# Kernel optimization log

Hardware: AMD Instinct MI355X
Metric: run time of the kernel (lower is better)

The kernel has to match this reference:

```python
import jax, jax.numpy as jnp
import numpy as np

B, S, HID = 1, 2048, 1024
NH, NKV, HD = 16, 4, 64
SCALING = 0.125  # attention_multiplier = 1/sqrt(head_dim)
ROPE_THETA = 10000.0
NEG_MIN = jnp.finfo(jnp.float32).min


def rotate_half(x):
    x1, x2 = jnp.split(x, 2, axis=-1)
    return jnp.concatenate([-x2, x1], axis=-1)


def setup_inputs() -> dict:
    key = jax.random.key(0)
    ks = jax.random.split(key, 6)
    hidden_states = jax.random.normal(ks[0], (B, S, HID), dtype=jnp.float32)
    # RoPE tables: [1, 1, S, HD]
    inv_freq = 1.0 / (ROPE_THETA ** (np.arange(0, HD, 2, dtype=np.float32) / HD))
    t = np.arange(S, dtype=np.float32)
    freqs = np.outer(t, inv_freq)                      # [S, HD/2]
    emb = np.concatenate([freqs, freqs], axis=-1)      # [S, HD]
    cos = jnp.asarray(np.cos(emb))[None, None]
    sin = jnp.asarray(np.sin(emb))[None, None]
    attention_mask = jnp.ones((B, S), dtype=bool)
    sc = 0.02
    Wq = jax.random.normal(ks[1], (HID, NH * HD), dtype=jnp.float32) * sc
    Wk = jax.random.normal(ks[2], (HID, NKV * HD), dtype=jnp.float32) * sc
    Wv = jax.random.normal(ks[3], (HID, NKV * HD), dtype=jnp.float32) * sc
    Wo = jax.random.normal(ks[4], (NH * HD, HID), dtype=jnp.float32) * sc
    return {"hidden_states": hidden_states, "cos": cos, "sin": sin,
            "attention_mask": attention_mask, "Wq": Wq, "Wk": Wk, "Wv": Wv, "Wo": Wo}


def reference(hidden_states, cos, sin, attention_mask, Wq, Wk, Wv, Wo):
    b, s, _ = hidden_states.shape
    # projections -> [B, H, S, D]
    q = (hidden_states @ Wq).reshape(b, s, NH, HD).transpose(0, 2, 1, 3)
    k = (hidden_states @ Wk).reshape(b, s, NKV, HD).transpose(0, 2, 1, 3)
    v = (hidden_states @ Wv).reshape(b, s, NKV, HD).transpose(0, 2, 1, 3)
    # RoPE (full head_dim rotation; cos/sin broadcast over batch/heads)
    q = q * cos + rotate_half(q) * sin
    k = k * cos + rotate_half(k) * sin
    # repeat_kv: expand kv heads to match query heads
    n_rep = NH // NKV
    k = jnp.repeat(k, n_rep, axis=1)
    v = jnp.repeat(v, n_rep, axis=1)
    # scores: [B, H, Sq, Sk]
    attn = jnp.einsum('bhqd,bhkd->bhqk', q, k) * SCALING
    mask = attention_mask[:, None, None, :].astype(attn.dtype)  # bool padding mask
    attn = attn + (1.0 - mask) * NEG_MIN
    attn = jax.nn.softmax(attn.astype(jnp.float32), axis=-1).astype(q.dtype)
    out = jnp.einsum('bhqk,bhkd->bhqd', attn, v)
    out = out.transpose(0, 2, 1, 3).reshape(b, s, NH * HD)
    return out @ Wo
```

## Files before the change

kernel.cpp:

```cpp
#include <hip/hip_runtime.h>
#include <stdint.h>

typedef __attribute__((ext_vector_type(8))) short short8;
typedef __attribute__((ext_vector_type(4))) short short4v;
typedef __attribute__((ext_vector_type(4))) float floatx4;

#define AS1 __attribute__((address_space(1)))
#define AS3 __attribute__((address_space(3)))

__device__ __forceinline__ void async16(const void* g, void* l) {
  __builtin_amdgcn_global_load_lds((const AS1 unsigned int*)g, (AS3 unsigned int*)l, 16, 0, 0);
}

__device__ __forceinline__ short f2bf(float f) {
  unsigned u = __float_as_uint(f);
  u = (u + 0x7FFF + ((u >> 16) & 1)) >> 16;
  return (short)u;
}

__device__ __forceinline__ void stage_sw(const short* src, int stride,
                                         short* tile, int cb, int lane) {
  int i = cb + lane;
  int r = i >> 3, j = i & 7;
  async16(src + (size_t)r * stride + ((j ^ (r & 7)) * 8), tile + cb * 8);
}
__device__ __forceinline__ int sw(int row, int c8) {
  return row * 64 + ((c8 ^ (row & 7)) * 8);
}

__global__ void k_f2bf(const float* __restrict__ in, short* __restrict__ out, int n) {
  int i = (blockIdx.x * 256 + threadIdx.x) * 4;
  if (i < n) {
    floatx4 v = *(const floatx4*)(in + i);
    short4v o;
    o.x = f2bf(v.x); o.y = f2bf(v.y); o.z = f2bf(v.z); o.w = f2bf(v.w);
    *(short4v*)(out + i) = o;
  }
}

__global__ void k_wt(const float* __restrict__ W, short* __restrict__ Wt, int K, int N) {
  __shared__ short t[32][33];
  int k0 = blockIdx.y * 32, n0 = blockIdx.x * 32;
  int tx = threadIdx.x, ty = threadIdx.y;
#pragma unroll
  for (int i = 0; i < 4; i++)
    t[ty + 8 * i][tx] = f2bf(W[(size_t)(k0 + ty + 8 * i) * N + n0 + tx]);
  __syncthreads();
#pragma unroll
  for (int i = 0; i < 4; i++)
    Wt[(size_t)(n0 + ty + 8 * i) * K + k0 + tx] = t[tx][ty + 8 * i];
}

__global__ void k_rope(const float* __restrict__ src, int stride, int off,
                       short* __restrict__ dst, const float* __restrict__ cosp,
                       const float* __restrict__ sinp, int H, int S, float scale) {
  int tid = blockIdx.x * 256 + threadIdx.x;
  int d = tid & 63;
  int h = (tid >> 6) % H;
  int s = tid / (64 * H);
  float v = src[(size_t)s * stride + off + h * 64 + d];
  float o = src[(size_t)s * stride + off + h * 64 + (d ^ 32)];
  float rot = (d < 32) ? -o : o;
  float c = cosp[s * 64 + d], sn = sinp[s * 64 + d];
  dst[((size_t)h * S + s) * 64 + d] = f2bf((v * c + rot * sn) * scale);
}

__global__ void k_vt(const float* __restrict__ src, short* __restrict__ Vt, int S) {
  __shared__ short t[32][33];
  int s0 = blockIdx.x * 32;
  int d0 = blockIdx.y * 32;
  int h = blockIdx.z;
  int tx = threadIdx.x, ty = threadIdx.y;
#pragma unroll
  for (int i = 0; i < 4; i++)
    t[ty + 8 * i][tx] = f2bf(src[(size_t)(s0 + ty + 8 * i) * 1536 + 1280 + h * 64 + d0 + tx]);
  __syncthreads();
#pragma unroll
  for (int i = 0; i < 4; i++)
    Vt[((size_t)h * 64 + d0 + ty + 8 * i) * S + s0 + tx] = t[tx][ty + 8 * i];
}

__global__ __launch_bounds__(256) void k_gemm(const short* __restrict__ A,
                                              const short* __restrict__ Bt,
                                              float* __restrict__ C,
                                              int M, int N, int K) {
  int tid = threadIdx.x;
  int w = tid >> 6, lane = tid & 63, quad = lane >> 4, l16 = lane & 15;
  __shared__ short As[64 * 64];
  __shared__ short Bs[128 * 64];
  const short* Ag = A + (size_t)(blockIdx.y * 64) * K;
  const short* Bg = Bt + (size_t)(blockIdx.x * 128) * K;
  floatx4 acc[4][2] = {};
  for (int kk = 0; kk < K; kk += 64) {
    __syncthreads();
#pragma unroll
    for (int t = 0; t < 2; t++) stage_sw(Ag + kk, K, As, (w * 2 + t) * 64, lane);
#pragma unroll
    for (int t = 0; t < 4; t++) stage_sw(Bg + kk, K, Bs, (w * 4 + t) * 64, lane);
    __syncthreads();
#pragma unroll
    for (int ks = 0; ks < 2; ks++) {
      short8 af[4], bfr[2];
#pragma unroll
      for (int i = 0; i < 4; i++)
        af[i] = *(const short8*)&As[sw(i * 16 + l16, ks * 4 + quad)];
#pragma unroll
      for (int j = 0; j < 2; j++)
        bfr[j] = *(const short8*)&Bs[sw(w * 32 + j * 16 + l16, ks * 4 + quad)];
#pragma unroll
      for (int i = 0; i < 4; i++)
#pragma unroll
        for (int j = 0; j < 2; j++)
          acc[i][j] = __builtin_amdgcn_mfma_f32_16x16x32_bf16(af[i], bfr[j], acc[i][j], 0, 0, 0);
    }
  }
#pragma unroll
  for (int i = 0; i < 4; i++)
#pragma unroll
    for (int j = 0; j < 2; j++)
#pragma unroll
      for (int r = 0; r < 4; r++) {
        int row = blockIdx.y * 64 + i * 16 + quad * 4 + r;
        int col = blockIdx.x * 128 + w * 32 + j * 16 + l16;
        C[(size_t)row * N + col] = acc[i][j][r];
      }
}

__global__ __launch_bounds__(256) void k_attn(const short* __restrict__ Qb,
                                              const short* __restrict__ Kb,
                                              const short* __restrict__ Vt,
                                              short* __restrict__ AOb) {
  int qt = blockIdx.x;
  int h = blockIdx.y;
  int kvh = h >> 2;
  int tid = threadIdx.x, w = tid >> 6, lane = tid & 63, quad = lane >> 4, l16 = lane & 15;
  __shared__ short Qs[4096];
  __shared__ short Ks[2][4096];
  __shared__ short Vs[2][4096];
  __shared__ short Ps[4][1152];
  const short* Qg = Qb + ((size_t)h * 2048 + qt * 64) * 64;
  const short* Kg0 = Kb + (size_t)kvh * 2048 * 64;
  const short* Vg0 = Vt + (size_t)kvh * 64 * 2048;
#pragma unroll
  for (int t = 0; t < 2; t++) stage_sw(Qg, 64, Qs, (w * 2 + t) * 64, lane);
#pragma unroll
  for (int t = 0; t < 2; t++) stage_sw(Kg0, 64, Ks[0], (w * 2 + t) * 64, lane);
#pragma unroll
  for (int t = 0; t < 2; t++) stage_sw(Vg0, 2048, Vs[0], (w * 2 + t) * 64, lane);
  short8 qf[2];
  floatx4 accO[4] = {};
  float lsum = 0.f;
  short* myPs = Ps[w];
  for (int kt = 0; kt < 32; kt++) {
    __syncthreads();
    if (kt == 0) {
      qf[0] = *(const short8*)&Qs[sw(w * 16 + l16, quad)];
      qf[1] = *(const short8*)&Qs[sw(w * 16 + l16, 4 + quad)];
    }
    if (kt + 1 < 32) {
      int nb = (kt + 1) & 1;
#pragma unroll
      for (int t = 0; t < 2; t++)
        stage_sw(Kg0 + (kt + 1) * 4096, 64, Ks[nb], (w * 2 + t) * 64, lane);
#pragma unroll
      for (int t = 0; t < 2; t++)
        stage_sw(Vg0 + (kt + 1) * 64, 2048, Vs[nb], (w * 2 + t) * 64, lane);
    }
    int cbuf = kt & 1;
    floatx4 accS[4] = {};
#pragma unroll
    for (int ks = 0; ks < 2; ks++)
#pragma unroll
      for (int mt = 0; mt < 4; mt++) {
        short8 af = *(const short8*)&Ks[cbuf][sw(mt * 16 + l16, ks * 4 + quad)];
        accS[mt] = __builtin_amdgcn_mfma_f32_16x16x32_bf16(af, qf[ks], accS[mt], 0, 0, 0);
      }
#pragma unroll
    for (int mt = 0; mt < 4; mt++) {
      short4v pk;
#pragma unroll
      for (int r = 0; r < 4; r++) {
        float p = __builtin_amdgcn_exp2f(accS[mt][r]);
        lsum += p;
        pk[r] = f2bf(p);
      }
      *(short4v*)&myPs[l16 * 72 + mt * 16 + quad * 4] = pk;
    }
    asm volatile("s_waitcnt lgkmcnt(0)" ::: "memory");
#pragma unroll
    for (int ks = 0; ks < 2; ks++) {
      short8 pf = *(const short8*)&myPs[l16 * 72 + ks * 32 + quad * 8];
#pragma unroll
      for (int dt = 0; dt < 4; dt++) {
        short8 vf = *(const short8*)&Vs[cbuf][sw(dt * 16 + l16, ks * 4 + quad)];
        accO[dt] = __builtin_amdgcn_mfma_f32_16x16x32_bf16(pf, vf, accO[dt], 0, 0, 0);
      }
    }
  }
  float ls = lsum;
  ls += __shfl_xor(ls, 16);
  ls += __shfl_xor(ls, 32);
  float inv[4];
#pragma unroll
  for (int r = 0; r < 4; r++)
    inv[r] = 1.0f / __shfl(ls, (lane & 48) | (quad * 4 + r));
#pragma unroll
  for (int dt = 0; dt < 4; dt++)
#pragma unroll
    for (int r = 0; r < 4; r++) {
      int srow = qt * 64 + w * 16 + quad * 4 + r;
      int col = h * 64 + dt * 16 + l16;
      AOb[(size_t)srow * 1024 + col] = f2bf(accO[dt][r] * inv[r]);
    }
}

extern "C" void kernel_launch(void* const* d_in, const int* in_sizes, int n_in,
                              void* d_out, int out_size, void* d_ws, size_t ws_size,
                              hipStream_t stream) {
  const float* X    = (const float*)d_in[0];
  const float* cosp = (const float*)d_in[1];
  const float* sinp = (const float*)d_in[2];
  const float* Wq = (const float*)d_in[4];
  const float* Wk = (const float*)d_in[5];
  const float* Wv = (const float*)d_in[6];
  const float* Wo = (const float*)d_in[7];
  float* out = (float*)d_out;

  short* Xb   = (short*)d_ws;
  short* Wqt  = Xb + 2097152;
  short* Wkt  = Wqt + 1048576;
  short* Wvt  = Wkt + 262144;
  short* Wot  = Wvt + 262144;
  float* QKVf = (float*)(Wot + 1048576);
  short* Qb2  = (short*)(QKVf + 3145728);
  short* Kb2  = Qb2 + 2097152;
  short* Vtb  = Kb2 + 524288;
  short* AOb  = Vtb + 524288;

  const float QSCALE = 0.125f * 1.44269504088896340736f;
  dim3 tb(32, 8);

  k_f2bf<<<2048, 256, 0, stream>>>(X, Xb, 2097152);
  k_wt<<<dim3(32, 32), tb, 0, stream>>>(Wq, Wqt, 1024, 1024);
  k_wt<<<dim3(8, 32), tb, 0, stream>>>(Wk, Wkt, 1024, 256);
  k_wt<<<dim3(8, 32), tb, 0, stream>>>(Wv, Wvt, 1024, 256);
  k_wt<<<dim3(32, 32), tb, 0, stream>>>(Wo, Wot, 1024, 1024);
  k_gemm<<<dim3(12, 32), 256, 0, stream>>>(Xb, Wqt, QKVf, 2048, 1536, 1024);
  k_rope<<<8192, 256, 0, stream>>>(QKVf, 1536, 0, Qb2, cosp, sinp, 16, 2048, QSCALE);
  k_rope<<<2048, 256, 0, stream>>>(QKVf, 1536, 1024, Kb2, cosp, sinp, 4, 2048, 1.0f);
  k_vt<<<dim3(64, 2, 4), tb, 0, stream>>>(QKVf, Vtb, 2048);
  k_attn<<<dim3(32, 16), 256, 0, stream>>>(Qb2, Kb2, Vtb, AOb);
  k_gemm<<<dim3(8, 32), 256, 0, stream>>>(AOb, Wot, out, 2048, 1024, 1024);
}
```

Before: 169.1 us.

## Fuse prep kernels, fold RoPE and V transpose into QKV GEMM, widen attention tiles

Merges the X conversion and four weight-transpose launches into one prep kernel. RoPE, Q scaling and the V transpose now run in the QKV GEMM epilogue, using a remapped B-tile row order so each lane holds both halves of a head dimension pair. This removes the fp32 QKV intermediate round trip and several launches. Attention now gives each wave 32 query rows loaded straight into registers, which halves the grid and K/V restaging per query but raises register pressure and lowers block count.

```diff
diff --git a/kernel.cpp b/kernel.cpp
--- a/kernel.cpp
+++ b/kernel.cpp
@@ -28,56 +28,107 @@
   return row * 64 + ((c8 ^ (row & 7)) * 8);
 }
 
-__global__ void k_f2bf(const float* __restrict__ in, short* __restrict__ out, int n) {
-  int i = (blockIdx.x * 256 + threadIdx.x) * 4;
-  if (i < n) {
-    floatx4 v = *(const floatx4*)(in + i);
+__global__ void k_prep(const float* __restrict__ X, const float* __restrict__ Wq,
+                       const float* __restrict__ Wk, const float* __restrict__ Wv,
+                       const float* __restrict__ Wo, short* __restrict__ Xb,
+                       short* __restrict__ Wqkvt, short* __restrict__ Wot) {
+  int b = blockIdx.x, tid = threadIdx.x;
+  if (b < 2048) {
+    int i = b * 1024 + tid * 4;
+    floatx4 v = *(const floatx4*)(X + i);
     short4v o;
     o.x = f2bf(v.x); o.y = f2bf(v.y); o.z = f2bf(v.z); o.w = f2bf(v.w);
-    *(short4v*)(out + i) = o;
-  }
-}
-
-__global__ void k_wt(const float* __restrict__ W, short* __restrict__ Wt, int K, int N) {
+    *(short4v*)(Xb + i) = o;
+    return;
+  }
+  const float* src; short* dst; int N, brel, rowoff;
+  if (b < 3072)      { src = Wq; dst = Wqkvt; N = 1024; brel = b - 2048; rowoff = 0; }
+  else if (b < 3328) { src = Wk; dst = Wqkvt; N = 256;  brel = b - 3072; rowoff = 1024; }
+  else if (b < 3584) { src = Wv; dst = Wqkvt; N = 256;  brel = b - 3328; rowoff = 1280; }
+  else               { src = Wo; dst = Wot;   N = 1024; brel = b - 3584; rowoff = 0; }
   __shared__ short t[32][33];
-  int k0 = blockIdx.y * 32, n0 = blockIdx.x * 32;
-  int tx = threadIdx.x, ty = threadIdx.y;
+  int nt = N >> 5;
+  int n0 = (brel % nt) * 32, k0 = (brel / nt) * 32;
+  int tx = tid & 31, ty = tid >> 5;
 #pragma unroll
   for (int i = 0; i < 4; i++)
-    t[ty + 8 * i][tx] = f2bf(W[(size_t)(k0 + ty + 8 * i) * N + n0 + tx]);
+    t[ty + 8 * i][tx] = f2bf(src[(size_t)(k0 + ty + 8 * i) * N + n0 + tx]);
   __syncthreads();
 #pragma unroll
   for (int i = 0; i < 4; i++)
-    Wt[(size_t)(n0 + ty + 8 * i) * K + k0 + tx] = t[tx][ty + 8 * i];
-}
-
-__global__ void k_rope(const float* __restrict__ src, int stride, int off,
-                       short* __restrict__ dst, const float* __restrict__ cosp,
-                       const float* __restrict__ sinp, int H, int S, float scale) {
-  int tid = blockIdx.x * 256 + threadIdx.x;
-  int d = tid & 63;
-  int h = (tid >> 6) % H;
-  int s = tid / (64 * H);
-  float v = src[(size_t)s * stride + off + h * 64 + d];
-  float o = src[(size_t)s * stride + off + h * 64 + (d ^ 32)];
-  float rot = (d < 32) ? -o : o;
-  float c = cosp[s * 64 + d], sn = sinp[s * 64 + d];
-  dst[((size_t)h * S + s) * 64 + d] = f2bf((v * c + rot * sn) * scale);
-}
-
-__global__ void k_vt(const float* __restrict__ src, short* __restrict__ Vt, int S) {
-  __shared__ short t[32][33];
-  int s0 = blockIdx.x * 32;
-  int d0 = blockIdx.y * 32;
-  int h = blockIdx.z;
-  int tx = threadIdx.x, ty = threadIdx.y;
-#pragma unroll
-  for (int i = 0; i < 4; i++)
-    t[ty + 8 * i][tx] = f2bf(src[(size_t)(s0 + ty + 8 * i) * 1536 + 1280 + h * 64 + d0 + tx]);
-  __syncthreads();
-#pragma unroll
-  for (int i = 0; i < 4; i++)
-    Vt[((size_t)h * 64 + d0 + ty + 8 * i) * S + s0 + tx] = t[tx][ty + 8 * i];
+    dst[(size_t)(rowoff + n0 + ty + 8 * i) * 1024 + k0 + tx] = t[tx][ty + 8 * i];
+}
+
+__global__ __launch_bounds__(256) void k_gemmqkv(const short* __restrict__ A,
+                                                 const short* __restrict__ Bt,
+                                                 short* __restrict__ Qb,
+                                                 short* __restrict__ Kb,
+                                                 short* __restrict__ Vtb,
+                                                 const float* __restrict__ cosp,
+                                                 const float* __restrict__ sinp,
+                                                 float qscale) {
+  int tid = threadIdx.x;
+  int w = tid >> 6, lane = tid & 63, quad = lane >> 4, l16 = lane & 15;
+  __shared__ short As[64 * 64];
+  __shared__ short Bs[128 * 64];
+  const int K = 1024;
+  const short* Ag = A + (size_t)(blockIdx.y * 64) * K;
+  const short* Bg = Bt + (size_t)(blockIdx.x * 128) * K;
+  int hw = w & 1;
+  int dlo = (w >> 1) * 16 + l16;
+  floatx4 acc[4][2] = {};
+  for (int kk = 0; kk < K; kk += 64) {
+    __syncthreads();
+#pragma unroll
+    for (int t = 0; t < 2; t++) stage_sw(Ag + kk, K, As, (w * 2 + t) * 64, lane);
+#pragma unroll
+    for (int t = 0; t < 4; t++) stage_sw(Bg + kk, K, Bs, (w * 4 + t) * 64, lane);
+    __syncthreads();
+#pragma unroll
+    for (int ks = 0; ks < 2; ks++) {
+      short8 af[4], bfr[2];
+#pragma unroll
+      for (int i = 0; i < 4; i++)
+        af[i] = *(const short8*)&As[sw(i * 16 + l16, ks * 4 + quad)];
+#pragma unroll
+      for (int j = 0; j < 2; j++)
+        bfr[j] = *(const short8*)&Bs[sw(hw * 64 + j * 32 + (w >> 1) * 16 + l16, ks * 4 + quad)];
+#pragma unroll
+      for (int i = 0; i < 4; i++)
+#pragma unroll
+        for (int j = 0; j < 2; j++)
+          acc[i][j] = __builtin_amdgcn_mfma_f32_16x16x32_bf16(af[i], bfr[j], acc[i][j], 0, 0, 0);
+    }
+  }
+  int bx = blockIdx.x, by = blockIdx.y;
+  if (bx < 10) {
+    short* dst; float scale;
+    if (bx < 8) { dst = Qb + (size_t)(bx * 2 + hw) * 2048 * 64; scale = qscale; }
+    else        { dst = Kb + (size_t)((bx - 8) * 2 + hw) * 2048 * 64; scale = 1.0f; }
+#pragma unroll
+    for (int i = 0; i < 4; i++)
+#pragma unroll
+      for (int r = 0; r < 4; r++) {
+        int s = by * 64 + i * 16 + quad * 4 + r;
+        float c = cosp[s * 64 + dlo], sn = sinp[s * 64 + dlo];
+        float v0 = acc[i][0][r], v1 = acc[i][1][r];
+        dst[(size_t)s * 64 + dlo]      = f2bf((v0 * c - v1 * sn) * scale);
+        dst[(size_t)s * 64 + 32 + dlo] = f2bf((v1 * c + v0 * sn) * scale);
+      }
+  } else {
+    short* dst = Vtb + (size_t)((bx - 10) * 2 + hw) * 64 * 2048;
+#pragma unroll
+    for (int j = 0; j < 2; j++) {
+      int d = j * 32 + dlo;
+#pragma unroll
+      for (int i = 0; i < 4; i++) {
+        short4v pk;
+#pragma unroll
+        for (int r = 0; r < 4; r++) pk[r] = f2bf(acc[i][j][r]);
+        *(short4v*)&dst[(size_t)d * 2048 + by * 64 + i * 16 + quad * 4] = pk;
+      }
+    }
+  }
 }
 
 __global__ __launch_bounds__(256) void k_gemm(const short* __restrict__ A,
@@ -134,29 +185,27 @@
   int h = blockIdx.y;
   int kvh = h >> 2;
   int tid = threadIdx.x, w = tid >> 6, lane = tid & 63, quad = lane >> 4, l16 = lane & 15;
-  __shared__ short Qs[4096];
   __shared__ short Ks[2][4096];
   __shared__ short Vs[2][4096];
-  __shared__ short Ps[4][1152];
-  const short* Qg = Qb + ((size_t)h * 2048 + qt * 64) * 64;
+  __shared__ short Ps[4][32 * 72];
+  const short* Qg = Qb + ((size_t)h * 2048 + qt * 128 + w * 32) * 64;
   const short* Kg0 = Kb + (size_t)kvh * 2048 * 64;
   const short* Vg0 = Vt + (size_t)kvh * 64 * 2048;
-#pragma unroll
-  for (int t = 0; t < 2; t++) stage_sw(Qg, 64, Qs, (w * 2 + t) * 64, lane);
+  short8 qf[2][2];
+#pragma unroll
+  for (int q2 = 0; q2 < 2; q2++)
+#pragma unroll
+    for (int ks = 0; ks < 2; ks++)
+      qf[q2][ks] = *(const short8*)(Qg + (q2 * 16 + l16) * 64 + ks * 32 + quad * 8);
 #pragma unroll
   for (int t = 0; t < 2; t++) stage_sw(Kg0, 64, Ks[0], (w * 2 + t) * 64, lane);
 #pragma unroll
   for (int t = 0; t < 2; t++) stage_sw(Vg0, 2048, Vs[0], (w * 2 + t) * 64, lane);
-  short8 qf[2];
-  floatx4 accO[4] = {};
-  float lsum = 0.f;
+  floatx4 accO[2][4] = {};
+  float lsum[2] = {0.f, 0.f};
   short* myPs = Ps[w];
   for (int kt = 0; kt < 32; kt++) {
     __syncthreads();
-    if (kt == 0) {
-      qf[0] = *(const short8*)&Qs[sw(w * 16 + l16, quad)];
-      qf[1] = *(const short8*)&Qs[sw(w * 16 + l16, 4 + quad)];
-    }
     if (kt + 1 < 32) {
       int nb = (kt + 1) & 1;
 #pragma unroll
@@ -167,51 +216,65 @@
         stage_sw(Vg0 + (kt + 1) * 64, 2048, Vs[nb], (w * 2 + t) * 64, lane);
     }
     int cbuf = kt & 1;
-    floatx4 accS[4] = {};
+    floatx4 accS[2][4] = {};
 #pragma unroll
     for (int ks = 0; ks < 2; ks++)
 #pragma unroll
       for (int mt = 0; mt < 4; mt++) {
         short8 af = *(const short8*)&Ks[cbuf][sw(mt * 16 + l16, ks * 4 + quad)];
-        accS[mt] = __builtin_amdgcn_mfma_f32_16x16x32_bf16(af, qf[ks], accS[mt], 0, 0, 0);
-      }
-#pragma unroll
-    for (int mt = 0; mt < 4; mt++) {
-      short4v pk;
-#pragma unroll
-      for (int r = 0; r < 4; r++) {
-        float p = __builtin_amdgcn_exp2f(accS[mt][r]);
-        lsum += p;
-        pk[r] = f2bf(p);
-      }
-      *(short4v*)&myPs[l16 * 72 + mt * 16 + quad * 4] = pk;
-    }
+#pragma unroll
+        for (int q2 = 0; q2 < 2; q2++)
+          accS[q2][mt] = __builtin_amdgcn_mfma_f32_16x16x32_bf16(af, qf[q2][ks], accS[q2][mt], 0, 0, 0);
+      }
+#pragma unroll
+    for (int q2 = 0; q2 < 2; q2++)
+#pragma unroll
+      for (int mt = 0; mt < 4; mt++) {
+        short4v pk;
+#pragma unroll
+        for (int r = 0; r < 4; r++) {
+          float p = __builtin_amdgcn_exp2f(accS[q2][mt][r]);
+          lsum[q2] += p;
+          pk[r] = f2bf(p);
+        }
+        *(short4v*)&myPs[(q2 * 16 + l16) * 72 + mt * 16 + quad * 4] = pk;
+      }
     asm volatile("s_waitcnt lgkmcnt(0)" ::: "memory");
 #pragma unroll
     for (int ks = 0; ks < 2; ks++) {
-      short8 pf = *(const short8*)&myPs[l16 * 72 + ks * 32 + quad * 8];
+      short8 pf[2];
+#pragma unroll
+      for (int q2 = 0; q2 < 2; q2++)
+        pf[q2] = *(const short8*)&myPs[(q2 * 16 + l16) * 72 + ks * 32 + quad * 8];
 #pragma unroll
       for (int dt = 0; dt < 4; dt++) {
         short8 vf = *(const short8*)&Vs[cbuf][sw(dt * 16 + l16, ks * 4 + quad)];
-        accO[dt] = __builtin_amdgcn_mfma_f32_16x16x32_bf16(pf, vf, accO[dt], 0, 0, 0);
-      }
-    }
-  }
-  float ls = lsum;
-  ls += __shfl_xor(ls, 16);
-  ls += __shfl_xor(ls, 32);
-  float inv[4];
-#pragma unroll
-  for (int r = 0; r < 4; r++)
-    inv[r] = 1.0f / __shfl(ls, (lane & 48) | (quad * 4 + r));
-#pragma unroll
-  for (int dt = 0; dt < 4; dt++)
-#pragma unroll
-    for (int r = 0; r < 4; r++) {
-      int srow = qt * 64 + w * 16 + quad * 4 + r;
-      int col = h * 64 + dt * 16 + l16;
-      AOb[(size_t)srow * 1024 + col] = f2bf(accO[dt][r] * inv[r]);
-    }
+#pragma unroll
+        for (int q2 = 0; q2 < 2; q2++)
+          accO[q2][dt] = __builtin_amdgcn_mfma_f32_16x16x32_bf16(pf[q2], vf, accO[q2][dt], 0, 0, 0);
+      }
+    }
+  }
+  float inv[2][4];
+#pragma unroll
+  for (int q2 = 0; q2 < 2; q2++) {
+    float ls = lsum[q2];
+    ls += __shfl_xor(ls, 16);
+    ls += __shfl_xor(ls, 32);
+#pragma unroll
+    for (int r = 0; r < 4; r++)
+      inv[q2][r] = 1.0f / __shfl(ls, (lane & 48) | (quad * 4 + r));
+  }
+#pragma unroll
+  for (int q2 = 0; q2 < 2; q2++)
+#pragma unroll
+    for (int dt = 0; dt < 4; dt++)
+#pragma unroll
+      for (int r = 0; r < 4; r++) {
+        int srow = qt * 128 + w * 32 + q2 * 16 + quad * 4 + r;
+        int col = h * 64 + dt * 16 + l16;
+        AOb[(size_t)srow * 1024 + col] = f2bf(accO[q2][dt][r] * inv[q2][r]);
+      }
 }
 
 extern "C" void kernel_launch(void* const* d_in, const int* in_sizes, int n_in,
@@ -226,29 +289,18 @@
   const float* Wo = (const float*)d_in[7];
   float* out = (float*)d_out;
 
-  short* Xb   = (short*)d_ws;
-  short* Wqt  = Xb + 2097152;
-  short* Wkt  = Wqt + 1048576;
-  short* Wvt  = Wkt + 262144;
-  short* Wot  = Wvt + 262144;
-  float* QKVf = (float*)(Wot + 1048576);
-  short* Qb2  = (short*)(QKVf + 3145728);
-  short* Kb2  = Qb2 + 2097152;
-  short* Vtb  = Kb2 + 524288;
-  short* AOb  = Vtb + 524288;
+  short* Xb    = (short*)d_ws;
+  short* Wqkvt = Xb + 2097152;
+  short* Wot   = Wqkvt + 1572864;
+  short* Qb2   = Wot + 1048576;
+  short* Kb2   = Qb2 + 2097152;
+  short* Vtb   = Kb2 + 524288;
+  short* AOb   = Vtb + 524288;
 
   const float QSCALE = 0.125f * 1.44269504088896340736f;
-  dim3 tb(32, 8);
-
-  k_f2bf<<<2048, 256, 0, stream>>>(X, Xb, 2097152);
-  k_wt<<<dim3(32, 32), tb, 0, stream>>>(Wq, Wqt, 1024, 1024);
-  k_wt<<<dim3(8, 32), tb, 0, stream>>>(Wk, Wkt, 1024, 256);
-  k_wt<<<dim3(8, 32), tb, 0, stream>>>(Wv, Wvt, 1024, 256);
-  k_wt<<<dim3(32, 32), tb, 0, stream>>>(Wo, Wot, 1024, 1024);
-  k_gemm<<<dim3(12, 32), 256, 0, stream>>>(Xb, Wqt, QKVf, 2048, 1536, 1024);
-  k_rope<<<8192, 256, 0, stream>>>(QKVf, 1536, 0, Qb2, cosp, sinp, 16, 2048, QSCALE);
-  k_rope<<<2048, 256, 0, stream>>>(QKVf, 1536, 1024, Kb2, cosp, sinp, 4, 2048, 1.0f);
-  k_vt<<<dim3(64, 2, 4), tb, 0, stream>>>(QKVf, Vtb, 2048);
-  k_attn<<<dim3(32, 16), 256, 0, stream>>>(Qb2, Kb2, Vtb, AOb);
+
+  k_prep<<<4608, 256, 0, stream>>>(X, Wq, Wk, Wv, Wo, Xb, Wqkvt, Wot);
+  k_gemmqkv<<<dim3(12, 32), 256, 0, stream>>>(Xb, Wqkvt, Qb2, Kb2, Vtb, cosp, sinp, QSCALE);
+  k_attn<<<dim3(16, 16), 256, 0, stream>>>(Qb2, Kb2, Vtb, AOb);
   k_gemm<<<dim3(8, 32), 256, 0, stream>>>(AOb, Wot, out, 2048, 1024, 1024);
 }
```

New measurement: 161.2 us. -4.6%, faster.
